# Optimization experiments

Measured on AMD Instinct MI355X. Metric: run time of the kernel, lower is better.

The kernel has to match this reference:

```python
import jax, jax.numpy as jnp
import numpy as np

B, S, TK, N = 16, 32, 128, 512  # batch, sentences, tokens/sentence, 2*hidden_dim


def setup_inputs() -> dict:
    key = jax.random.key(0)
    ks = jax.random.split(key, 10)
    h = jax.random.normal(ks[0], (B, S, TK, N), dtype=jnp.float32)
    s_t_hat = jax.random.normal(ks[1], (B, N), dtype=jnp.float32)
    coverage = jax.random.uniform(ks[2], (B, S, TK), dtype=jnp.float32)
    # binary padding mask (mostly ones)
    enc_padding_mask = (jax.random.uniform(ks[3], (B, S, TK)) > 0.1).astype(jnp.float32)
    beta = jax.random.uniform(ks[4], (B, S), dtype=jnp.float32)
    sc = 1.0 / np.sqrt(N).astype(np.float32)
    W_h = jax.random.normal(ks[5], (N, N), dtype=jnp.float32) * sc   # Linear(N,N,bias=False)
    W_c = jax.random.normal(ks[6], (N,), dtype=jnp.float32)          # Linear(1,N,bias=False) weight[:,0]
    W_d = jax.random.normal(ks[7], (N, N), dtype=jnp.float32) * sc   # decode_proj weight
    b_d = jax.random.normal(ks[8], (N,), dtype=jnp.float32) * sc     # decode_proj bias
    v = jax.random.normal(ks[9], (N,), dtype=jnp.float32) * sc       # v weight[0]
    return {"s_t_hat": s_t_hat, "h": h, "coverage": coverage,
            "enc_padding_mask": enc_padding_mask, "beta": beta,
            "W_h": W_h, "W_c": W_c, "W_d": W_d, "b_d": b_d, "v": v}


def reference(s_t_hat, h, coverage, enc_padding_mask, beta, W_h, W_c, W_d, b_d, v):
    b, s, t_k, n = h.shape
    # encoder features: (b,s,t_k,n) @ W_h^T
    encoder_feature = jnp.einsum('bstn,mn->bstm', h, W_h)
    # decoder projection, broadcast over (s, t_k)
    dec_fea = s_t_hat @ W_d.T + b_d                              # (b, n)
    att_features = encoder_feature + dec_fea[:, None, None, :]
    # coverage feature: Linear(1, n) applied to coverage scalar
    att_features = att_features + coverage[..., None] * W_c     # (b,s,t_k,n)
    # scalar scores via v()
    scores = jnp.einsum('bstn,n->bst', jnp.tanh(att_features), v)
    # beta-weighted scores, flatten sentence/token dims
    weighted = (beta[:, :, None] * scores).reshape(b, s * t_k)
    mask_flat = enc_padding_mask.reshape(b, s * t_k)
    attn_ = jax.nn.softmax(weighted, axis=1) * mask_flat
    attn_dist = attn_ / attn_.sum(axis=1, keepdims=True)         # (b, s*t_k)
    # context vector
    c_t = jnp.einsum('bl,bln->bn', attn_dist, h.reshape(b, s * t_k, n))
    coverage_new = coverage + attn_dist.reshape(b, s, t_k)
    return c_t, attn_dist, coverage_new
```

## Files before the change

### kernel.cpp

```cpp
#include <hip/hip_runtime.h>
#include <hip/hip_bf16.h>

#define BB   16
#define SS   32
#define TKK  128
#define NN   512
#define LPB  4096
#define RPB  64

using bf16x8 = __attribute__((ext_vector_type(8))) __bf16;
using f32x4  = __attribute__((ext_vector_type(4))) float;

__device__ inline unsigned pack_bf16(float a, float b) {
  unsigned ua = __float_as_uint(a);
  unsigned ub = __float_as_uint(b);
  ua = (ua + 0x7FFFu + ((ua >> 16) & 1u)) >> 16;
  ub = (ub + 0x7FFFu + ((ub >> 16) & 1u)) >> 16;
  return ua | (ub << 16);
}

__device__ inline float tanh_fast(float x) {
  float e = __expf(2.0f * x);
  return 1.0f - 2.0f * __builtin_amdgcn_rcpf(e + 1.0f);
}

__global__ void prep_wpack(const float* __restrict__ W_h, uint4* __restrict__ Wpack) {
  int idx  = blockIdx.x * 256 + threadIdx.x;
  int lane = idx & 63;
  int ks   = (idx >> 6) & 15;
  int mt   = idx >> 10;
  int m    = mt * 16 + (lane & 15);
  int k0   = ks * 32 + ((lane >> 4) << 2);
  const float* wr = W_h + m * NN;
  float a0 = wr[k0 + 0],  a1 = wr[k0 + 1],  a2 = wr[k0 + 2],  a3 = wr[k0 + 3];
  float b0 = wr[k0 + 16], b1 = wr[k0 + 17], b2 = wr[k0 + 18], b3 = wr[k0 + 19];
  uint4 o;
  o.x = pack_bf16(a0, a1); o.y = pack_bf16(a2, a3);
  o.z = pack_bf16(b0, b1); o.w = pack_bf16(b2, b3);
  Wpack[idx] = o;
}

__global__ void prep_decfea(const float* __restrict__ s_t_hat,
                            const float* __restrict__ W_d,
                            const float* __restrict__ b_d,
                            float* __restrict__ decfea) {
  int idx = blockIdx.x * 256 + threadIdx.x;
  int b = idx >> 9, m = idx & 511;
  const float4* sp = reinterpret_cast<const float4*>(s_t_hat + b * NN);
  const float4* wp = reinterpret_cast<const float4*>(W_d + m * NN);
  float acc = 0.f;
  #pragma unroll 8
  for (int i = 0; i < NN / 4; ++i) {
    float4 a = sp[i], w = wp[i];
    acc += a.x * w.x + a.y * w.y + a.z * w.z + a.w * w.w;
  }
  decfea[idx] = acc + b_d[m];
}

__global__ __launch_bounds__(256, 2)
void score_kernel(const float* __restrict__ h,
                  const float* __restrict__ coverage,
                  const float* __restrict__ beta,
                  const float* __restrict__ W_c,
                  const float* __restrict__ v,
                  const uint4* __restrict__ Wpack,
                  const float* __restrict__ decfea,
                  float* __restrict__ weighted) {
  __shared__ __align__(16) unsigned short Afrag[RPB * NN];
  int tid  = threadIdx.x;
  int rb   = blockIdx.x;
  int bidx = rb >> 6;
  const float* hblk = h + (size_t)rb * RPB * NN;

  uint2* Af2 = reinterpret_cast<uint2*>(Afrag);
  #pragma unroll 8
  for (int i = 0; i < 32; ++i) {
    int u     = i * 256 + tid;
    int g     = u & 1;
    int lane6 = (u >> 1) & 63;
    int ksrt  = u >> 7;
    int row   = ((ksrt >> 4) << 4) + (lane6 & 15);
    int k0    = (ksrt & 15) * 32 + g * 16 + ((lane6 >> 4) << 2);
    float4 hv = *reinterpret_cast<const float4*>(hblk + row * NN + k0);
    uint2 p;
    p.x = pack_bf16(hv.x, hv.y);
    p.y = pack_bf16(hv.z, hv.w);
    Af2[u] = p;
  }
  __syncthreads();

  int lane = tid & 63;
  int w    = tid >> 6;

  f32x4 acc[8][4];
  const f32x4 zz = {0.f, 0.f, 0.f, 0.f};
  #pragma unroll
  for (int q = 0; q < 8; ++q)
    #pragma unroll
    for (int rt = 0; rt < 4; ++rt) acc[q][rt] = zz;

  const bf16x8* Afv = reinterpret_cast<const bf16x8*>(Afrag);
  const bf16x8* Bv  = reinterpret_cast<const bf16x8*>(Wpack);

  for (int ks = 0; ks < 16; ++ks) {
    bf16x8 af[4];
    #pragma unroll
    for (int rt = 0; rt < 4; ++rt)
      af[rt] = Afv[(rt * 16 + ks) * 64 + lane];
    #pragma unroll
    for (int q = 0; q < 8; ++q) {
      int mt = w * 8 + q;
      bf16x8 bf = Bv[(mt * 16 + ks) * 64 + lane];
      #pragma unroll
      for (int rt = 0; rt < 4; ++rt)
        acc[q][rt] = __builtin_amdgcn_mfma_f32_16x16x32_bf16(af[rt], bf, acc[q][rt], 0, 0, 0);
    }
  }

  int col = lane & 15;
  int rhi = (lane >> 4) << 2;
  float cv[4][4];
  #pragma unroll
  for (int rt = 0; rt < 4; ++rt)
    #pragma unroll
    for (int r = 0; r < 4; ++r)
      cv[rt][r] = coverage[rb * RPB + rt * 16 + rhi + r];

  float sc[4][4] = {};
  #pragma unroll
  for (int q = 0; q < 8; ++q) {
    int m = (w * 8 + q) * 16 + col;
    float dv = decfea[bidx * NN + m];
    float wc = W_c[m];
    float vv = v[m];
    #pragma unroll
    for (int rt = 0; rt < 4; ++rt)
      #pragma unroll
      for (int r = 0; r < 4; ++r) {
        float x = acc[q][rt][r] + dv + cv[rt][r] * wc;
        sc[rt][r] += vv * tanh_fast(x);
      }
  }
  #pragma unroll
  for (int rt = 0; rt < 4; ++rt)
    #pragma unroll
    for (int r = 0; r < 4; ++r) {
      float s = sc[rt][r];
      s += __shfl_xor(s, 1);
      s += __shfl_xor(s, 2);
      s += __shfl_xor(s, 4);
      s += __shfl_xor(s, 8);
      sc[rt][r] = s;
    }

  __syncthreads();
  float* scorebuf = reinterpret_cast<float*>(Afrag);
  if (col == 0) {
    #pragma unroll
    for (int rt = 0; rt < 4; ++rt)
      #pragma unroll
      for (int r = 0; r < 4; ++r)
        scorebuf[w * 64 + rt * 16 + rhi + r] = sc[rt][r];
  }
  __syncthreads();
  if (tid < 64) {
    float total = scorebuf[tid] + scorebuf[64 + tid] + scorebuf[128 + tid] + scorebuf[192 + tid];
    int gl = rb * RPB + tid;
    int lb = gl & (LPB - 1);
    int s  = lb >> 7;
    weighted[bidx * LPB + lb] = beta[bidx * SS + s] * total;
  }
}

__global__ void softmax_kernel(const float* __restrict__ coverage,
                               const float* __restrict__ mask,
                               float* __restrict__ out) {
  int b = blockIdx.x;
  int t = threadIdx.x;
  float* ct   = out;
  float* attn = out + 8192;
  float* covn = out + 8192 + 65536;

  ct[b * NN + t] = 0.f;
  ct[b * NN + 256 + t] = 0.f;

  float wv[16];
  float mx = -1e30f;
  #pragma unroll
  for (int i = 0; i < 16; ++i) {
    wv[i] = attn[b * LPB + i * 256 + t];
    mx = fmaxf(mx, wv[i]);
  }
  __shared__ float redm[4], reds[4];
  mx = fmaxf(mx, __shfl_xor(mx, 1));
  mx = fmaxf(mx, __shfl_xor(mx, 2));
  mx = fmaxf(mx, __shfl_xor(mx, 4));
  mx = fmaxf(mx, __shfl_xor(mx, 8));
  mx = fmaxf(mx, __shfl_xor(mx, 16));
  mx = fmaxf(mx, __shfl_xor(mx, 32));
  if ((t & 63) == 0) redm[t >> 6] = mx;
  __syncthreads();
  mx = fmaxf(fmaxf(redm[0], redm[1]), fmaxf(redm[2], redm[3]));

  float e[16];
  float sum = 0.f;
  #pragma unroll
  for (int i = 0; i < 16; ++i) {
    e[i] = __expf(wv[i] - mx) * mask[b * LPB + i * 256 + t];
    sum += e[i];
  }
  sum += __shfl_xor(sum, 1);
  sum += __shfl_xor(sum, 2);
  sum += __shfl_xor(sum, 4);
  sum += __shfl_xor(sum, 8);
  sum += __shfl_xor(sum, 16);
  sum += __shfl_xor(sum, 32);
  if ((t & 63) == 0) reds[t >> 6] = sum;
  __syncthreads();
  sum = reds[0] + reds[1] + reds[2] + reds[3];
  float inv = 1.0f / sum;
  #pragma unroll
  for (int i = 0; i < 16; ++i) {
    int l = i * 256 + t;
    float a = e[i] * inv;
    attn[b * LPB + l] = a;
    covn[b * LPB + l] = coverage[b * LPB + l] + a;
  }
}

__global__ void ct_kernel(const float* __restrict__ h, float* __restrict__ out) {
  int blk   = blockIdx.x;
  int b     = blk >> 6;
  int chunk = blk & 63;
  int t     = threadIdx.x;
  const float* attn = out + 8192 + b * LPB + chunk * 64;
  __shared__ float as_[64];
  if (t < 64) as_[t] = attn[t];
  __syncthreads();
  const float* hp = h + (size_t)(b * LPB + chunk * 64) * NN;
  float a0 = 0.f, a1 = 0.f;
  #pragma unroll 4
  for (int r = 0; r < 64; ++r) {
    float2 hv = *reinterpret_cast<const float2*>(hp + r * NN + t * 2);
    float av = as_[r];
    a0 += av * hv.x;
    a1 += av * hv.y;
  }
  atomicAdd(&out[b * NN + t * 2],     a0);
  atomicAdd(&out[b * NN + t * 2 + 1], a1);
}

extern "C" void kernel_launch(void* const* d_in, const int* in_sizes, int n_in,
                              void* d_out, int out_size, void* d_ws, size_t ws_size,
                              hipStream_t stream) {
  const float* s_t_hat  = (const float*)d_in[0];
  const float* h        = (const float*)d_in[1];
  const float* coverage = (const float*)d_in[2];
  const float* mask     = (const float*)d_in[3];
  const float* beta     = (const float*)d_in[4];
  const float* W_h      = (const float*)d_in[5];
  const float* W_c      = (const float*)d_in[6];
  const float* W_d      = (const float*)d_in[7];
  const float* b_d      = (const float*)d_in[8];
  const float* v        = (const float*)d_in[9];
  float* out = (float*)d_out;

  uint4* Wpack   = (uint4*)d_ws;
  float* decfea  = out + 8192 + 65536;
  float* weighted = out + 8192;

  prep_wpack <<<128, 256, 0, stream>>>(W_h, Wpack);
  prep_decfea<<<32, 256, 0, stream>>>(s_t_hat, W_d, b_d, decfea);
  score_kernel<<<1024, 256, 0, stream>>>(h, coverage, beta, W_c, v, Wpack, decfea, weighted);
  softmax_kernel<<<16, 256, 0, stream>>>(coverage, mask, out);
  ct_kernel<<<1024, 256, 0, stream>>>(h, out);
}
```

Measured before the change: 116.5 us.

## Split score GEMM across 8 waves, prefetch W fragments, merge prep kernels

The score kernel now runs with 512 threads (8 waves) per block. Each wave handles 4 output column tiles instead of 8, which halves the accumulator registers and aims to raise occupancy via launch_bounds(512,4). W_h bf16 fragments are software-prefetched one k-step ahead to hide global load latency. The two prep kernels are fused into a single launch to save launch overhead. The 64KB LDS tile per block may still cap blocks per CU, so the occupancy gain depends on LDS limits.

```diff
diff --git a/kernel.cpp b/kernel.cpp
--- a/kernel.cpp
+++ b/kernel.cpp
@@ -24,40 +24,41 @@
   return 1.0f - 2.0f * __builtin_amdgcn_rcpf(e + 1.0f);
 }
 
-__global__ void prep_wpack(const float* __restrict__ W_h, uint4* __restrict__ Wpack) {
-  int idx  = blockIdx.x * 256 + threadIdx.x;
-  int lane = idx & 63;
-  int ks   = (idx >> 6) & 15;
-  int mt   = idx >> 10;
-  int m    = mt * 16 + (lane & 15);
-  int k0   = ks * 32 + ((lane >> 4) << 2);
-  const float* wr = W_h + m * NN;
-  float a0 = wr[k0 + 0],  a1 = wr[k0 + 1],  a2 = wr[k0 + 2],  a3 = wr[k0 + 3];
-  float b0 = wr[k0 + 16], b1 = wr[k0 + 17], b2 = wr[k0 + 18], b3 = wr[k0 + 19];
-  uint4 o;
-  o.x = pack_bf16(a0, a1); o.y = pack_bf16(a2, a3);
-  o.z = pack_bf16(b0, b1); o.w = pack_bf16(b2, b3);
-  Wpack[idx] = o;
-}
-
-__global__ void prep_decfea(const float* __restrict__ s_t_hat,
+__global__ void prep_kernel(const float* __restrict__ W_h, uint4* __restrict__ Wpack,
+                            const float* __restrict__ s_t_hat,
                             const float* __restrict__ W_d,
                             const float* __restrict__ b_d,
                             float* __restrict__ decfea) {
-  int idx = blockIdx.x * 256 + threadIdx.x;
-  int b = idx >> 9, m = idx & 511;
-  const float4* sp = reinterpret_cast<const float4*>(s_t_hat + b * NN);
-  const float4* wp = reinterpret_cast<const float4*>(W_d + m * NN);
-  float acc = 0.f;
-  #pragma unroll 8
-  for (int i = 0; i < NN / 4; ++i) {
-    float4 a = sp[i], w = wp[i];
-    acc += a.x * w.x + a.y * w.y + a.z * w.z + a.w * w.w;
-  }
-  decfea[idx] = acc + b_d[m];
-}
-
-__global__ __launch_bounds__(256, 2)
+  if (blockIdx.x < 128) {
+    int idx  = blockIdx.x * 256 + threadIdx.x;
+    int lane = idx & 63;
+    int ks   = (idx >> 6) & 15;
+    int mt   = idx >> 10;
+    int m    = mt * 16 + (lane & 15);
+    int k0   = ks * 32 + ((lane >> 4) << 2);
+    const float* wr = W_h + m * NN;
+    float a0 = wr[k0 + 0],  a1 = wr[k0 + 1],  a2 = wr[k0 + 2],  a3 = wr[k0 + 3];
+    float b0 = wr[k0 + 16], b1 = wr[k0 + 17], b2 = wr[k0 + 18], b3 = wr[k0 + 19];
+    uint4 o;
+    o.x = pack_bf16(a0, a1); o.y = pack_bf16(a2, a3);
+    o.z = pack_bf16(b0, b1); o.w = pack_bf16(b2, b3);
+    Wpack[idx] = o;
+  } else {
+    int idx = (blockIdx.x - 128) * 256 + threadIdx.x;
+    int b = idx >> 9, m = idx & 511;
+    const float4* sp = reinterpret_cast<const float4*>(s_t_hat + b * NN);
+    const float4* wp = reinterpret_cast<const float4*>(W_d + m * NN);
+    float acc = 0.f;
+    #pragma unroll 8
+    for (int i = 0; i < NN / 4; ++i) {
+      float4 a = sp[i], w = wp[i];
+      acc += a.x * w.x + a.y * w.y + a.z * w.z + a.w * w.w;
+    }
+    decfea[idx] = acc + b_d[m];
+  }
+}
+
+__global__ __launch_bounds__(512, 4)
 void score_kernel(const float* __restrict__ h,
                   const float* __restrict__ coverage,
                   const float* __restrict__ beta,
@@ -73,9 +74,9 @@
   const float* hblk = h + (size_t)rb * RPB * NN;
 
   uint2* Af2 = reinterpret_cast<uint2*>(Afrag);
-  #pragma unroll 8
-  for (int i = 0; i < 32; ++i) {
-    int u     = i * 256 + tid;
+  #pragma unroll
+  for (int i = 0; i < 16; ++i) {
+    int u     = i * 512 + tid;
     int g     = u & 1;
     int lane6 = (u >> 1) & 63;
     int ksrt  = u >> 7;
@@ -92,29 +93,38 @@
   int lane = tid & 63;
   int w    = tid >> 6;
 
-  f32x4 acc[8][4];
+  f32x4 acc[4][4];
   const f32x4 zz = {0.f, 0.f, 0.f, 0.f};
   #pragma unroll
-  for (int q = 0; q < 8; ++q)
+  for (int q = 0; q < 4; ++q)
     #pragma unroll
     for (int rt = 0; rt < 4; ++rt) acc[q][rt] = zz;
 
   const bf16x8* Afv = reinterpret_cast<const bf16x8*>(Afrag);
-  const bf16x8* Bv  = reinterpret_cast<const bf16x8*>(Wpack);
-
+  const bf16x8* Bv  = reinterpret_cast<const bf16x8*>(Wpack) + (size_t)(w * 4) * 16 * 64 + lane;
+
+  bf16x8 bf[4];
+  #pragma unroll
+  for (int q = 0; q < 4; ++q)
+    bf[q] = Bv[(q * 16 + 0) * 64];
   for (int ks = 0; ks < 16; ++ks) {
     bf16x8 af[4];
     #pragma unroll
     for (int rt = 0; rt < 4; ++rt)
       af[rt] = Afv[(rt * 16 + ks) * 64 + lane];
-    #pragma unroll
-    for (int q = 0; q < 8; ++q) {
-      int mt = w * 8 + q;
-      bf16x8 bf = Bv[(mt * 16 + ks) * 64 + lane];
+    bf16x8 bn[4];
+    if (ks < 15) {
+      #pragma unroll
+      for (int q = 0; q < 4; ++q)
+        bn[q] = Bv[(q * 16 + ks + 1) * 64];
+    }
+    #pragma unroll
+    for (int q = 0; q < 4; ++q)
       #pragma unroll
       for (int rt = 0; rt < 4; ++rt)
-        acc[q][rt] = __builtin_amdgcn_mfma_f32_16x16x32_bf16(af[rt], bf, acc[q][rt], 0, 0, 0);
-    }
+        acc[q][rt] = __builtin_amdgcn_mfma_f32_16x16x32_bf16(af[rt], bf[q], acc[q][rt], 0, 0, 0);
+    #pragma unroll
+    for (int q = 0; q < 4; ++q) bf[q] = bn[q];
   }
 
   int col = lane & 15;
@@ -128,8 +138,8 @@
 
   float sc[4][4] = {};
   #pragma unroll
-  for (int q = 0; q < 8; ++q) {
-    int m = (w * 8 + q) * 16 + col;
+  for (int q = 0; q < 4; ++q) {
+    int m = (w * 4 + q) * 16 + col;
     float dv = decfea[bidx * NN + m];
     float wc = W_c[m];
     float vv = v[m];
@@ -160,11 +170,13 @@
     for (int rt = 0; rt < 4; ++rt)
       #pragma unroll
       for (int r = 0; r < 4; ++r)
-        scorebuf[w * 64 + rt * 16 + rhi + r] = sc[rt][r];
-  }
-  __syncthreads();
-  if (tid < 64) {
-    float total = scorebuf[tid] + scorebuf[64 + tid] + scorebuf[128 + tid] + scorebuf[192 + tid];
+        scorebuf[w * RPB + rt * 16 + rhi + r] = sc[rt][r];
+  }
+  __syncthreads();
+  if (tid < RPB) {
+    float total = 0.f;
+    #pragma unroll
+    for (int ww = 0; ww < 8; ++ww) total += scorebuf[ww * RPB + tid];
     int gl = rb * RPB + tid;
     int lb = gl & (LPB - 1);
     int s  = lb >> 7;
@@ -265,13 +277,12 @@
   const float* v        = (const float*)d_in[9];
   float* out = (float*)d_out;
 
-  uint4* Wpack   = (uint4*)d_ws;
-  float* decfea  = out + 8192 + 65536;
+  uint4* Wpack    = (uint4*)d_ws;
+  float* decfea   = out + 8192 + 65536;
   float* weighted = out + 8192;
 
-  prep_wpack <<<128, 256, 0, stream>>>(W_h, Wpack);
-  prep_decfea<<<32, 256, 0, stream>>>(s_t_hat, W_d, b_d, decfea);
-  score_kernel<<<1024, 256, 0, stream>>>(h, coverage, beta, W_c, v, Wpack, decfea, weighted);
+  prep_kernel <<<160, 256, 0, stream>>>(W_h, Wpack, s_t_hat, W_d, b_d, decfea);
+  score_kernel<<<1024, 512, 0, stream>>>(h, coverage, beta, W_c, v, Wpack, decfea, weighted);
   softmax_kernel<<<16, 256, 0, stream>>>(coverage, mask, out);
   ct_kernel<<<1024, 256, 0, stream>>>(h, out);
 }
```

After: 105.1 us. -9.7%, faster.
